# Kernel tuning notes

Hardware: AMD Instinct MI355X
Metric: run time of the kernel (lower is better)

## Reference

```python
import jax, jax.numpy as jnp
import numpy as np

IN_DIM = 3
OUT_DIM = 3
HSI_DIM = 31
MIN_BAND = 400.0
MAX_BAND = 700.0
N_BAND = 31  # == HSI_DIM so the indexed write fills every column
BN_EPS = 1e-5


def setup_inputs() -> dict:
    key = jax.random.key(0)
    ks = jax.random.split(key, 8)
    B, H, W = 16, 256, 256
    x = jax.random.uniform(ks[0], (B, H, W, IN_DIM), jnp.float32)
    x_hsi = jax.random.uniform(ks[1], (B, H, W, HSI_DIM), jnp.float32)
    conv_w = jax.random.normal(ks[2], (64, IN_DIM, 3, 3), jnp.float32) * 0.1
    conv_b = jax.random.normal(ks[3], (64,), jnp.float32) * 0.1
    bn_w = 1.0 + jax.random.normal(ks[4], (64,), jnp.float32) * 0.1
    bn_b = jax.random.normal(ks[5], (64,), jnp.float32) * 0.1
    fc_w = jax.random.normal(ks[6], (OUT_DIM + 2, 64), jnp.float32) * 0.1
    fc_b = jax.random.normal(ks[7], (OUT_DIM + 2,), jnp.float32) * 0.1
    return {"x": x, "x_hsi": x_hsi, "conv_w": conv_w, "conv_b": conv_b,
            "bn_w": bn_w, "bn_b": bn_b, "fc_w": fc_w, "fc_b": fc_b}


def _voltage_net(x, conv_w, conv_b, bn_w, bn_b, fc_w, fc_b):
    # x: (B, H, W, 3) channels-last -> NCHW
    xp = jnp.transpose(x, (0, 3, 1, 2))
    y = jax.lax.conv_general_dilated(
        xp, conv_w, window_strides=(1, 1), padding='SAME',
        dimension_numbers=('NCHW', 'OIHW', 'NCHW')) + conv_b[None, :, None, None]
    # BatchNorm2d (training-mode batch statistics, biased variance)
    mu = y.mean(axis=(0, 2, 3))
    var = y.var(axis=(0, 2, 3))
    y = (y - mu[None, :, None, None]) * jax.lax.rsqrt(var + BN_EPS)[None, :, None, None]
    y = y * bn_w[None, :, None, None] + bn_b[None, :, None, None]
    y = jax.nn.relu(y)
    feat = y.mean(axis=(2, 3))                      # AdaptiveAvgPool2d(1) -> (B, 64)
    raw = feat @ fc_w.T + fc_b                      # (B, out_dim + 2)
    mn = raw.min(axis=1, keepdims=True)
    mx = raw.max(axis=1, keepdims=True)
    norm = (raw - mn) / (mx - mn + 1e-8)
    mid = jnp.sort(norm, axis=1)[:, 1:-1]           # drop smallest & largest
    return mid * 10.0                               # (B, out_dim) voltages


def reference(x, x_hsi, conv_w, conv_b, bn_w, bn_b, fc_w, fc_b):
    voltages = _voltage_net(x, conv_w, conv_b, bn_w, bn_b, fc_w, fc_b)  # (B, C)
    # Vectorized Lyot SRF (replaces per-batch python loop); nBand == hsi_dim
    n = jnp.arange(N_BAND, dtype=jnp.float32)
    band = MIN_BAND + (MAX_BAND - MIN_BAND) * n / N_BAND                # (A,)
    cos_part = jnp.cos(2.0 * jnp.pi * (-0.01) / voltages)               # (B, C)
    srf = (0.5 - 0.5 * cos_part)[:, :, None] / (band[None, None, :] * 1e-6)  # (B, C, A)
    # contract hyperspectral bands: (B,C,A) x (B,H,W,A) -> (B,H,W,C)
    return jnp.einsum('bca,bpqa->bpqc', srf, x_hsi)
```

## Files before the change

kernel.cpp:

```cpp
#include <hip/hip_runtime.h>
#include <hip/hip_bf16.h>
#include <math.h>

#define BB 16
#define HH 256
#define WW 256

#define OFF_CHSUM 0
#define OFF_CHSQ  64
#define OFF_FEAT  256

#define PAN_DW (7 * 776)

typedef __attribute__((ext_vector_type(8))) short bf16x8;
typedef __attribute__((ext_vector_type(4))) float f32x4;

union BFu { __hip_bfloat16 h; short s; };
union ABu { bf16x8 v; unsigned u[4]; };

__device__ __forceinline__ unsigned packsplit(float v) {
    BFu hi; hi.h = __float2bfloat16(v);
    float rs = v - __bfloat162float(hi.h);
    BFu lo; lo.h = __float2bfloat16(rs);
    return (unsigned)(unsigned short)hi.s | ((unsigned)(unsigned short)lo.s << 16);
}

__global__ void k_init(float* __restrict__ ws) {
    int i = blockIdx.x * 256 + threadIdx.x;
    if (i < 1280) ws[i] = 0.f;
}

template <int MODE>
__global__ __launch_bounds__(256) void k_conv3(const float* __restrict__ x,
                                               const float* __restrict__ cw,
                                               const float* __restrict__ cb,
                                               const float* __restrict__ bnw,
                                               const float* __restrict__ bnb,
                                               float* __restrict__ ws) {
    __shared__ unsigned lds[PAN_DW];
    __shared__ float s_w[1728];
    __shared__ float s_b[64];
    __shared__ float red[4][4][16][2];
    const int t    = threadIdx.x;
    const int lane = t & 63;
    const int wv   = t >> 6;
    const int b    = blockIdx.y;
    const int r0   = blockIdx.x * 4;
    const int mrow = lane & 15;
    const int s    = lane >> 4;
    const bool s3  = (s == 3);
    const float* __restrict__ xb = x + (size_t)b * (HH * WW * 3);

    for (int i = t; i < 1728; i += 256) s_w[i] = cw[i];
    if (t < 64) s_b[t] = cb[t];

    for (int e = t; e < 6 * 774; e += 256) {
        const int l = e / 774, j = e - l * 774;
        const int gr = r0 - 1 + l, gcf = j - 3;
        const bool ok = ((unsigned)gr < 256u) && ((unsigned)gcf < 768u);
        int off = gr * 768 + gcf;
        off = ok ? off : 0;
        float v = xb[off];
        v = ok ? v : 0.f;
        lds[l * 776 + j] = packsplit(v);
    }
    for (int j = t; j < 776; j += 256) lds[6 * 776 + j] = 0x3F80u;

    float av[4], bvv[4];
#pragma unroll
    for (int n = 0; n < 4; ++n) {
        const int ch = n * 16 + mrow;
        if (MODE == 1) {
            const float invN = 1.f / 1048576.f;
            const float mu = ws[OFF_CHSUM + ch] * invN;
            const float vr = ws[OFF_CHSQ + ch] * invN - mu * mu;
            const float rs = rsqrtf(vr + 1e-5f);
            av[n]  = rs * bnw[ch];
            bvv[n] = bnb[ch] - mu * av[n];
        } else { av[n] = 1.f; bvv[n] = 0.f; }
    }

    int off8[8];
#pragma unroll
    for (int e = 0; e < 8; ++e) {
        if (!s3)        off8[e] = (wv + s) * 776 + e;
        else if (e < 3) off8[e] = (wv + e) * 776 + 8;
        else            off8[e] = 6 * 776 + e;
    }
    const int mrow3 = mrow * 3;

    __syncthreads();

    bf16x8 bh[4], bl[4];
#pragma unroll
    for (int n = 0; n < 4; ++n) {
        const int ch = n * 16 + mrow;
#pragma unroll
        for (int e = 0; e < 8; ++e) {
            float w = 0.f;
            if (!s3) {
                w = s_w[ch * 27 + (e % 3) * 9 + s * 3 + (e / 3)];
            } else if (e < 3) {
                w = s_w[ch * 27 + 18 + e * 3 + 2];
            } else if (e == 3) {
                w = s_b[ch];
            }
            if (MODE == 1) {
                w *= av[n];
                if (s3 && e == 3) w += bvv[n];
            }
            BFu hi; hi.h = __float2bfloat16(w);
            const float rs2 = w - __bfloat162float(hi.h);
            BFu lo; lo.h = __float2bfloat16(rs2);
            bh[n][e] = hi.s;
            bl[n][e] = lo.s;
        }
    }

    float a0[4] = {0.f, 0.f, 0.f, 0.f};
    float a1[4] = {0.f, 0.f, 0.f, 0.f};

#define GATHER(W, CS)                                                   \
    {                                                                   \
        const int c3 = (CS) * 48 + mrow3;                               \
        W[0] = lds[off8[0] + c3]; W[1] = lds[off8[1] + c3];             \
        W[2] = lds[off8[2] + c3]; W[3] = lds[off8[3] + c3];             \
        W[4] = lds[off8[4] + c3]; W[5] = lds[off8[5] + c3];             \
        W[6] = lds[off8[6] + c3]; W[7] = lds[off8[7] + c3];             \
    }
#define COMPUTE(W)                                                      \
    {                                                                   \
        ABu ua, ul;                                                     \
        ua.u[0] = (W[0] & 0xFFFFu) | (W[1] << 16);                      \
        ua.u[1] = (W[2] & 0xFFFFu) | (W[3] << 16);                      \
        ua.u[2] = (W[4] & 0xFFFFu) | (W[5] << 16);                      \
        ua.u[3] = (W[6] & 0xFFFFu) | (W[7] << 16);                      \
        ul.u[0] = (W[0] >> 16) | (W[1] & 0xFFFF0000u);                  \
        ul.u[1] = (W[2] >> 16) | (W[3] & 0xFFFF0000u);                  \
        ul.u[2] = (W[4] >> 16) | (W[5] & 0xFFFF0000u);                  \
        ul.u[3] = (W[6] >> 16) | (W[7] & 0xFFFF0000u);                  \
        const bf16x8 ah = ua.v, al = ul.v;                              \
        _Pragma("unroll")                                               \
        for (int n = 0; n < 4; ++n) {                                   \
            f32x4 acc = {0.f, 0.f, 0.f, 0.f};                           \
            acc = __builtin_amdgcn_mfma_f32_16x16x32_bf16(ah, bl[n], acc, 0, 0, 0); \
            acc = __builtin_amdgcn_mfma_f32_16x16x32_bf16(al, bh[n], acc, 0, 0, 0); \
            acc = __builtin_amdgcn_mfma_f32_16x16x32_bf16(ah, bh[n], acc, 0, 0, 0); \
            _Pragma("unroll")                                           \
            for (int i = 0; i < 4; ++i) {                               \
                const float y = acc[i];                                 \
                if (MODE == 0) { a0[n] += y; a1[n] = fmaf(y, y, a1[n]); } \
                else { a0[n] += fmaxf(y, 0.f); }                        \
            }                                                           \
        }                                                               \
    }

    {
        unsigned Wa[8], Wb[8];
        GATHER(Wa, 0)
        GATHER(Wb, 1)  COMPUTE(Wa)
        GATHER(Wa, 2)  COMPUTE(Wb)
        GATHER(Wb, 3)  COMPUTE(Wa)
        GATHER(Wa, 4)  COMPUTE(Wb)
        GATHER(Wb, 5)  COMPUTE(Wa)
        GATHER(Wa, 6)  COMPUTE(Wb)
        GATHER(Wb, 7)  COMPUTE(Wa)
        GATHER(Wa, 8)  COMPUTE(Wb)
        GATHER(Wb, 9)  COMPUTE(Wa)
        GATHER(Wa, 10) COMPUTE(Wb)
        GATHER(Wb, 11) COMPUTE(Wa)
        GATHER(Wa, 12) COMPUTE(Wb)
        GATHER(Wb, 13) COMPUTE(Wa)
        GATHER(Wa, 14) COMPUTE(Wb)
        GATHER(Wb, 15) COMPUTE(Wa)
        COMPUTE(Wb)
    }
#undef GATHER
#undef COMPUTE

#pragma unroll
    for (int n = 0; n < 4; ++n) {
        a0[n] += __shfl_xor(a0[n], 16);
        a0[n] += __shfl_xor(a0[n], 32);
        if (MODE == 0) {
            a1[n] += __shfl_xor(a1[n], 16);
            a1[n] += __shfl_xor(a1[n], 32);
        }
    }
    if (lane < 16) {
#pragma unroll
        for (int n = 0; n < 4; ++n) {
            red[wv][n][lane][0] = a0[n];
            red[wv][n][lane][1] = (MODE == 0) ? a1[n] : 0.f;
        }
    }
    __syncthreads();
    if (t < 64) {
        const int n = t >> 4, m = t & 15;
        const float S = red[0][n][m][0] + red[1][n][m][0] + red[2][n][m][0] + red[3][n][m][0];
        if (MODE == 0) {
            const float Q = red[0][n][m][1] + red[1][n][m][1] + red[2][n][m][1] + red[3][n][m][1];
            atomicAdd(&ws[OFF_CHSUM + t], S);
            atomicAdd(&ws[OFF_CHSQ + t], Q);
        } else {
            atomicAdd(&ws[OFF_FEAT + b * 64 + t], S);
        }
    }
}

__global__ __launch_bounds__(256) void k_final(const float* __restrict__ fcw,
                                               const float* __restrict__ fcb,
                                               const float* __restrict__ ws,
                                               const float* __restrict__ xh,
                                               float* __restrict__ out) {
    __shared__ float s_x[256 * 31];
    __shared__ float s_g[32];
    __shared__ float s_raw[5];
    __shared__ float sp[3];
    __shared__ float s_o[768];
    const int t = threadIdx.x;
    const int blk = blockIdx.x;
    const int b = blk >> 8;
    const size_t pix0 = (size_t)blk << 8;

    if (t < 31) {
        const float band = 400.f + (300.f * (float)t) / 31.f;
        s_g[t] = 1.f / (band * 1e-6f);
    }
    if (t >= 32 && t < 37) {
        const int j = t - 32;
        const float inv = 1.f / 65536.f;
        float a = fcb[j];
        for (int c = 0; c < 64; ++c)
            a = fmaf(fcw[j * 64 + c], ws[OFF_FEAT + b * 64 + c] * inv, a);
        s_raw[j] = a;
    }
    const float4* xg = (const float4*)(xh + pix0 * 31);
    float4* sx4 = (float4*)s_x;
#pragma unroll
    for (int i = 0; i < 8; ++i) {
        int idx = t + (i << 8);
        if (idx < 1984) sx4[idx] = xg[idx];
    }
    __syncthreads();
    if (t == 0) {
        float raw[5];
#pragma unroll
        for (int j = 0; j < 5; ++j) raw[j] = s_raw[j];
#define CS(i, j)                              \
        {                                     \
            float lo = fminf(raw[i], raw[j]); \
            float hi = fmaxf(raw[i], raw[j]); \
            raw[i] = lo;                      \
            raw[j] = hi;                      \
        }
        CS(0, 1) CS(3, 4) CS(2, 4) CS(2, 3) CS(0, 3) CS(0, 2) CS(1, 4) CS(1, 3) CS(1, 2)
#undef CS
        const float mn = raw[0], mx = raw[4];
        const float sc = 10.f / (mx - mn + 1e-8f);
#pragma unroll
        for (int c2 = 0; c2 < 3; ++c2) {
            const float v = (raw[1 + c2] - mn) * sc;
            const float sh = sinf(0.031415926535897934f / v);
            sp[c2] = sh * sh;
        }
    }
    __syncthreads();
    float z = 0.f;
    const float* px = s_x + t * 31;
#pragma unroll
    for (int a = 0; a < 31; ++a) z = fmaf(px[a], s_g[a], z);
    s_o[t * 3 + 0] = sp[0] * z;
    s_o[t * 3 + 1] = sp[1] * z;
    s_o[t * 3 + 2] = sp[2] * z;
    __syncthreads();
    float* ob = out + pix0 * 3;
#pragma unroll
    for (int i = 0; i < 3; ++i) ob[t + (i << 8)] = s_o[t + (i << 8)];
}

extern "C" void kernel_launch(void* const* d_in, const int* in_sizes, int n_in,
                              void* d_out, int out_size, void* d_ws, size_t ws_size,
                              hipStream_t stream) {
    const float* x    = (const float*)d_in[0];
    const float* xhsi = (const float*)d_in[1];
    const float* cw   = (const float*)d_in[2];
    const float* cb   = (const float*)d_in[3];
    const float* bnw  = (const float*)d_in[4];
    const float* bnb  = (const float*)d_in[5];
    const float* fcw  = (const float*)d_in[6];
    const float* fcb  = (const float*)d_in[7];
    float* out = (float*)d_out;
    float* ws  = (float*)d_ws;

    hipLaunchKernelGGL(k_init, dim3(5), dim3(256), 0, stream, ws);
    hipLaunchKernelGGL((k_conv3<0>), dim3(64, 16), dim3(256), 0, stream,
                       x, cw, cb, bnw, bnb, ws);
    hipLaunchKernelGGL((k_conv3<1>), dim3(64, 16), dim3(256), 0, stream,
                       x, cw, cb, bnw, bnb, ws);
    hipLaunchKernelGGL(k_final, dim3(4096), dim3(256), 0, stream, fcw, fcb, ws, xhsi, out);
}
```

Baseline: 92.15 us.

## Split conv row panels into column halves across a third grid dimension

Each conv block now handles half of the image width, selected by blockIdx.z. This doubles the grid and halves the LDS panel row stride. The gather/compute pipeline is rebuilt as a three-buffer rotation over 8 column chunks instead of a two-buffer rotation over 16. The goal is more blocks for occupancy, smaller LDS per block and deeper load-ahead, at the cost of loading duplicated halo columns and running more atomic reductions per channel.

```diff
diff --git a/kernel.cpp b/kernel.cpp
--- a/kernel.cpp
+++ b/kernel.cpp
@@ -10,7 +10,8 @@
 #define OFF_CHSQ  64
 #define OFF_FEAT  256
 
-#define PAN_DW (7 * 776)
+#define PROW 392
+#define PAN_DW (7 * PROW)
 
 typedef __attribute__((ext_vector_type(8))) short bf16x8;
 typedef __attribute__((ext_vector_type(4))) float f32x4;
@@ -31,7 +32,7 @@
 }
 
 template <int MODE>
-__global__ __launch_bounds__(256) void k_conv3(const float* __restrict__ x,
+__global__ __launch_bounds__(256) void k_conv4(const float* __restrict__ x,
                                                const float* __restrict__ cw,
                                                const float* __restrict__ cb,
                                                const float* __restrict__ bnw,
@@ -46,6 +47,7 @@
     const int wv   = t >> 6;
     const int b    = blockIdx.y;
     const int r0   = blockIdx.x * 4;
+    const int z    = blockIdx.z;
     const int mrow = lane & 15;
     const int s    = lane >> 4;
     const bool s3  = (s == 3);
@@ -54,17 +56,20 @@
     for (int i = t; i < 1728; i += 256) s_w[i] = cw[i];
     if (t < 64) s_b[t] = cb[t];
 
-    for (int e = t; e < 6 * 774; e += 256) {
-        const int l = e / 774, j = e - l * 774;
-        const int gr = r0 - 1 + l, gcf = j - 3;
-        const bool ok = ((unsigned)gr < 256u) && ((unsigned)gcf < 768u);
-        int off = gr * 768 + gcf;
-        off = ok ? off : 0;
-        float v = xb[off];
-        v = ok ? v : 0.f;
-        lds[l * 776 + j] = packsplit(v);
-    }
-    for (int j = t; j < 776; j += 256) lds[6 * 776 + j] = 0x3F80u;
+    {
+        const int g0 = 384 * z - 3;
+        for (int e = t; e < 6 * 390; e += 256) {
+            const int l = e / 390, j = e - l * 390;
+            const int gr = r0 - 1 + l, gcf = g0 + j;
+            const bool ok = ((unsigned)gr < 256u) && ((unsigned)gcf < 768u);
+            int off = gr * 768 + gcf;
+            off = ok ? off : 0;
+            float v = xb[off];
+            v = ok ? v : 0.f;
+            lds[l * PROW + j] = packsplit(v);
+        }
+        for (int j = t; j < PROW; j += 256) lds[6 * PROW + j] = 0x3F80u;
+    }
 
     float av[4], bvv[4];
 #pragma unroll
@@ -83,9 +88,9 @@
     int off8[8];
 #pragma unroll
     for (int e = 0; e < 8; ++e) {
-        if (!s3)        off8[e] = (wv + s) * 776 + e;
-        else if (e < 3) off8[e] = (wv + e) * 776 + 8;
-        else            off8[e] = 6 * 776 + e;
+        if (!s3)        off8[e] = (wv + s) * PROW + e;
+        else if (e < 3) off8[e] = (wv + e) * PROW + 8;
+        else            off8[e] = 6 * PROW + e;
     }
     const int mrow3 = mrow * 3;
 
@@ -156,23 +161,15 @@
     }
 
     {
-        unsigned Wa[8], Wb[8];
-        GATHER(Wa, 0)
-        GATHER(Wb, 1)  COMPUTE(Wa)
-        GATHER(Wa, 2)  COMPUTE(Wb)
-        GATHER(Wb, 3)  COMPUTE(Wa)
-        GATHER(Wa, 4)  COMPUTE(Wb)
-        GATHER(Wb, 5)  COMPUTE(Wa)
-        GATHER(Wa, 6)  COMPUTE(Wb)
-        GATHER(Wb, 7)  COMPUTE(Wa)
-        GATHER(Wa, 8)  COMPUTE(Wb)
-        GATHER(Wb, 9)  COMPUTE(Wa)
-        GATHER(Wa, 10) COMPUTE(Wb)
-        GATHER(Wb, 11) COMPUTE(Wa)
-        GATHER(Wa, 12) COMPUTE(Wb)
-        GATHER(Wb, 13) COMPUTE(Wa)
-        GATHER(Wa, 14) COMPUTE(Wb)
-        GATHER(Wb, 15) COMPUTE(Wa)
+        unsigned Wa[8], Wb[8], Wc[8];
+        GATHER(Wa, 0) GATHER(Wb, 1)
+        COMPUTE(Wa)   GATHER(Wc, 2)
+        COMPUTE(Wb)   GATHER(Wa, 3)
+        COMPUTE(Wc)   GATHER(Wb, 4)
+        COMPUTE(Wa)   GATHER(Wc, 5)
+        COMPUTE(Wb)   GATHER(Wa, 6)
+        COMPUTE(Wc)   GATHER(Wb, 7)
+        COMPUTE(Wa)
         COMPUTE(Wb)
     }
 #undef GATHER
@@ -294,9 +291,9 @@
     float* ws  = (float*)d_ws;
 
     hipLaunchKernelGGL(k_init, dim3(5), dim3(256), 0, stream, ws);
-    hipLaunchKernelGGL((k_conv3<0>), dim3(64, 16), dim3(256), 0, stream,
+    hipLaunchKernelGGL((k_conv4<0>), dim3(64, 16, 2), dim3(256), 0, stream,
                        x, cw, cb, bnw, bnb, ws);
-    hipLaunchKernelGGL((k_conv3<1>), dim3(64, 16), dim3(256), 0, stream,
+    hipLaunchKernelGGL((k_conv4<1>), dim3(64, 16, 2), dim3(256), 0, stream,
                        x, cw, cb, bnw, bnb, ws);
     hipLaunchKernelGGL(k_final, dim3(4096), dim3(256), 0, stream, fcw, fcb, ws, xhsi, out);
 }
```

New measurement: 122.2 us. 1.33x slower.

## Compute hyperspectral band contraction inside first conv pass to overlap with stats

Applied to the files above, without the earlier changes.

The per-pixel weighted sum over the 31 hyperspectral bands does not depend on the voltages. It is moved into extra blocks of the first conv-statistics launch, which write a scalar z per pixel to workspace. The final kernel then only reads z and scales it by the three per-batch factors. This overlaps the large x_hsi read with the compute-bound conv stats pass and leaves the final kernel light, at the cost of an extra 4 MB workspace write and read and a shared-memory union that enlarges the conv kernel's LDS layout.

```diff
diff --git a/kernel.cpp b/kernel.cpp
--- a/kernel.cpp
+++ b/kernel.cpp
@@ -9,8 +9,14 @@
 #define OFF_CHSUM 0
 #define OFF_CHSQ  64
 #define OFF_FEAT  256
-
-#define PAN_DW (7 * 776)
+#define OFF_Z     2048
+
+#define SM_PAN   0
+#define SM_W     21728
+#define SM_B     28640
+#define SM_RED   28896
+#define SM_G     31744
+#define SM_BYTES 32000
 
 typedef __attribute__((ext_vector_type(8))) short bf16x8;
 typedef __attribute__((ext_vector_type(4))) float f32x4;
@@ -31,20 +37,53 @@
 }
 
 template <int MODE>
-__global__ __launch_bounds__(256) void k_conv3(const float* __restrict__ x,
+__global__ __launch_bounds__(256) void k_convz(const float* __restrict__ x,
+                                               const float* __restrict__ xh,
                                                const float* __restrict__ cw,
                                                const float* __restrict__ cb,
                                                const float* __restrict__ bnw,
                                                const float* __restrict__ bnb,
                                                float* __restrict__ ws) {
-    __shared__ unsigned lds[PAN_DW];
-    __shared__ float s_w[1728];
-    __shared__ float s_b[64];
-    __shared__ float red[4][4][16][2];
-    const int t    = threadIdx.x;
+    __shared__ __align__(16) char smem[SM_BYTES];
+    const int t = threadIdx.x;
+    const int b = blockIdx.y;
+
+    if (blockIdx.x >= 64) {
+        float* s_x = (float*)smem;
+        float* s_g = (float*)(smem + SM_G);
+        const int zx = blockIdx.x - 64;
+        if (t < 31) {
+            const float band = 400.f + (300.f * (float)t) / 31.f;
+            s_g[t] = 1.f / (band * 1e-6f);
+        }
+#pragma unroll 1
+        for (int c = 0; c < 8; ++c) {
+            const size_t pxbase = (size_t)b * 65536 + zx * 2048 + c * 256;
+            const float4* xg = (const float4*)(xh + pxbase * 31);
+            float4* sx4 = (float4*)s_x;
+#pragma unroll
+            for (int i = 0; i < 8; ++i) {
+                int idx = t + (i << 8);
+                if (idx < 1984) sx4[idx] = xg[idx];
+            }
+            __syncthreads();
+            float z = 0.f;
+            const float* px = s_x + t * 31;
+#pragma unroll
+            for (int a = 0; a < 31; ++a) z = fmaf(px[a], s_g[a], z);
+            ws[OFF_Z + pxbase + t] = z;
+            __syncthreads();
+        }
+        return;
+    }
+
+    unsigned* pan32 = (unsigned*)smem;
+    float* s_w = (float*)(smem + SM_W);
+    float* s_b = (float*)(smem + SM_B);
+    float (*red)[4][16][2] = (float (*)[4][16][2])(smem + SM_RED);
+
     const int lane = t & 63;
     const int wv   = t >> 6;
-    const int b    = blockIdx.y;
     const int r0   = blockIdx.x * 4;
     const int mrow = lane & 15;
     const int s    = lane >> 4;
@@ -62,9 +101,9 @@
         off = ok ? off : 0;
         float v = xb[off];
         v = ok ? v : 0.f;
-        lds[l * 776 + j] = packsplit(v);
-    }
-    for (int j = t; j < 776; j += 256) lds[6 * 776 + j] = 0x3F80u;
+        pan32[l * 776 + j] = packsplit(v);
+    }
+    for (int j = t; j < 776; j += 256) pan32[6 * 776 + j] = 0x3F80u;
 
     float av[4], bvv[4];
 #pragma unroll
@@ -123,10 +162,10 @@
 #define GATHER(W, CS)                                                   \
     {                                                                   \
         const int c3 = (CS) * 48 + mrow3;                               \
-        W[0] = lds[off8[0] + c3]; W[1] = lds[off8[1] + c3];             \
-        W[2] = lds[off8[2] + c3]; W[3] = lds[off8[3] + c3];             \
-        W[4] = lds[off8[4] + c3]; W[5] = lds[off8[5] + c3];             \
-        W[6] = lds[off8[6] + c3]; W[7] = lds[off8[7] + c3];             \
+        W[0] = pan32[off8[0] + c3]; W[1] = pan32[off8[1] + c3];         \
+        W[2] = pan32[off8[2] + c3]; W[3] = pan32[off8[3] + c3];         \
+        W[4] = pan32[off8[4] + c3]; W[5] = pan32[off8[5] + c3];         \
+        W[6] = pan32[off8[6] + c3]; W[7] = pan32[off8[7] + c3];         \
     }
 #define COMPUTE(W)                                                      \
     {                                                                   \
@@ -208,13 +247,10 @@
     }
 }
 
-__global__ __launch_bounds__(256) void k_final(const float* __restrict__ fcw,
-                                               const float* __restrict__ fcb,
-                                               const float* __restrict__ ws,
-                                               const float* __restrict__ xh,
-                                               float* __restrict__ out) {
-    __shared__ float s_x[256 * 31];
-    __shared__ float s_g[32];
+__global__ __launch_bounds__(256) void k_final2(const float* __restrict__ fcw,
+                                                const float* __restrict__ fcb,
+                                                const float* __restrict__ ws,
+                                                float* __restrict__ out) {
     __shared__ float s_raw[5];
     __shared__ float sp[3];
     __shared__ float s_o[768];
@@ -223,24 +259,12 @@
     const int b = blk >> 8;
     const size_t pix0 = (size_t)blk << 8;
 
-    if (t < 31) {
-        const float band = 400.f + (300.f * (float)t) / 31.f;
-        s_g[t] = 1.f / (band * 1e-6f);
-    }
-    if (t >= 32 && t < 37) {
-        const int j = t - 32;
+    if (t < 5) {
         const float inv = 1.f / 65536.f;
-        float a = fcb[j];
+        float a = fcb[t];
         for (int c = 0; c < 64; ++c)
-            a = fmaf(fcw[j * 64 + c], ws[OFF_FEAT + b * 64 + c] * inv, a);
-        s_raw[j] = a;
-    }
-    const float4* xg = (const float4*)(xh + pix0 * 31);
-    float4* sx4 = (float4*)s_x;
-#pragma unroll
-    for (int i = 0; i < 8; ++i) {
-        int idx = t + (i << 8);
-        if (idx < 1984) sx4[idx] = xg[idx];
+            a = fmaf(fcw[t * 64 + c], ws[OFF_FEAT + b * 64 + c] * inv, a);
+        s_raw[t] = a;
     }
     __syncthreads();
     if (t == 0) {
@@ -266,10 +290,7 @@
         }
     }
     __syncthreads();
-    float z = 0.f;
-    const float* px = s_x + t * 31;
-#pragma unroll
-    for (int a = 0; a < 31; ++a) z = fmaf(px[a], s_g[a], z);
+    const float z = ws[OFF_Z + pix0 + t];
     s_o[t * 3 + 0] = sp[0] * z;
     s_o[t * 3 + 1] = sp[1] * z;
     s_o[t * 3 + 2] = sp[2] * z;
@@ -294,9 +315,9 @@
     float* ws  = (float*)d_ws;
 
     hipLaunchKernelGGL(k_init, dim3(5), dim3(256), 0, stream, ws);
-    hipLaunchKernelGGL((k_conv3<0>), dim3(64, 16), dim3(256), 0, stream,
-                       x, cw, cb, bnw, bnb, ws);
-    hipLaunchKernelGGL((k_conv3<1>), dim3(64, 16), dim3(256), 0, stream,
-                       x, cw, cb, bnw, bnb, ws);
-    hipLaunchKernelGGL(k_final, dim3(4096), dim3(256), 0, stream, fcw, fcb, ws, xhsi, out);
-}
+    hipLaunchKernelGGL((k_convz<0>), dim3(96, 16), dim3(256), 0, stream,
+                       x, xhsi, cw, cb, bnw, bnb, ws);
+    hipLaunchKernelGGL((k_convz<1>), dim3(64, 16), dim3(256), 0, stream,
+                       x, xhsi, cw, cb, bnw, bnb, ws);
+    hipLaunchKernelGGL(k_final2, dim3(4096), dim3(256), 0, stream, fcw, fcb, ws, out);
+}
```

Result: faster. 83.90 us (-8.9%).
